# Kernel optimization log

Hardware: AMD Instinct MI355X
Metric: run time of the kernel (lower is better)

Reference implementation:

```python
import jax, jax.numpy as jnp
import numpy as np

N, B, D, K_IN, P = 64, 256, 1792, 35, 10
EPS = 1e-5


def setup_inputs() -> dict:
    key = jax.random.key(0)
    ks = jax.random.split(key, 8)
    s_tok = 1.0 / np.sqrt(K_IN)
    s_net = 1.0 / np.sqrt(D)
    return {
        "X": jax.random.normal(ks[0], (N, B, D), dtype=jnp.float32),
        "task_id": jax.random.normal(ks[1], (B, K_IN), dtype=jnp.float32),
        # tokens: Linear(35, 10*1792)
        "W_tok": jax.random.uniform(ks[2], (P * D, K_IN), jnp.float32, -s_tok, s_tok),
        "b_tok": jax.random.uniform(ks[3], (P * D,), jnp.float32, -s_tok, s_tok),
        # ptokens: Linear(35, 1792)
        "W_ptok": jax.random.uniform(ks[4], (D, K_IN), jnp.float32, -s_tok, s_tok),
        "b_ptok": jax.random.uniform(ks[5], (D,), jnp.float32, -s_tok, s_tok),
        # LayerNorm(1792)
        "gamma": jnp.ones((D,), jnp.float32),
        "beta": jnp.zeros((D,), jnp.float32),
        # net: Linear(1792, 10)
        "W_net": jax.random.uniform(ks[6], (P, D), jnp.float32, -s_net, s_net),
        "b_net": jax.random.uniform(ks[7], (P,), jnp.float32, -s_net, s_net),
    }


def _layernorm(x, gamma, beta):
    mu = jnp.mean(x, axis=-1, keepdims=True)
    var = jnp.mean(jnp.square(x - mu), axis=-1, keepdims=True)
    return (x - mu) * jax.lax.rsqrt(var + EPS) * gamma + beta


def reference(X, task_id, W_tok, b_tok, W_ptok, b_ptok, gamma, beta, W_net, b_net):
    # ptokens(task_id): (b, D); identical across n, so compute once and broadcast.
    ptok = task_id @ W_ptok.T + b_ptok                       # (b, D)
    task_token = _layernorm(ptok[None, :, :] + X, gamma, beta)  # (n, b, D)
    # net -> sigmoid: per-token mixing weights over P prompts.
    weight = jax.nn.sigmoid(task_token @ W_net.T + b_net)    # (n, b, P)
    # tokens(task_id): (b, P, D); identical across n, broadcast in einsum.
    prompt_bank = (task_id @ W_tok.T + b_tok).reshape(B, P, D)  # (b, P, D)
    prompt = jnp.einsum("nbp,bpd->nbd", weight, prompt_bank)  # (n, b, D)
    return X + prompt
```

## Files before the change

kernel.cpp:

```cpp
#include <hip/hip_runtime.h>
#include <hip/hip_bf16.h>

#define NN 64
#define BB 256
#define DD 1792
#define KK 35
#define PP 10
#define DQ 448
#define GR 8
#define NGRP 28

__device__ __forceinline__ float group16_sum_dpp(float x) {
    asm("v_add_f32_dpp %0, %0, %0 row_shr:1 row_mask:0xf bank_mask:0xf bound_ctrl:0" : "+v"(x));
    asm("v_add_f32_dpp %0, %0, %0 row_shr:2 row_mask:0xf bank_mask:0xf bound_ctrl:0" : "+v"(x));
    asm("v_add_f32_dpp %0, %0, %0 row_shr:4 row_mask:0xf bank_mask:0xf bound_ctrl:0" : "+v"(x));
    asm("v_add_f32_dpp %0, %0, %0 row_shr:8 row_mask:0xf bank_mask:0xf bound_ctrl:0" : "+v"(x));
    return x;
}

#define PIN4(v) asm volatile("" : "+v"(v.x), "+v"(v.y), "+v"(v.z), "+v"(v.w))
#define PIN1(s) asm volatile("" : "+v"(s))

__global__ void prep_gf(const float* __restrict__ gamma, const float* __restrict__ beta,
                        const float* __restrict__ Wnet, const float* __restrict__ bnet,
                        float* __restrict__ GF, float* __restrict__ SG, float* __restrict__ ZC) {
    const int p = blockIdx.x;
    const int tid = threadIdx.x;
    float sg = 0.f, sb = 0.f;
#pragma unroll
    for (int j = 0; j < 7; ++j) {
        int d = j * 256 + tid;
        float wv = Wnet[p * DD + d];
        float g = gamma[d] * wv;
        GF[p * DD + d] = g;
        sg += g;
        sb += beta[d] * wv;
    }
#pragma unroll
    for (int off = 32; off > 0; off >>= 1) {
        sg += __shfl_xor(sg, off);
        sb += __shfl_xor(sb, off);
    }
    __shared__ float rs[4][2];
    if ((tid & 63) == 0) { rs[tid >> 6][0] = sg; rs[tid >> 6][1] = sb; }
    __syncthreads();
    if (tid == 0) {
        float a = 0.f, c = 0.f;
#pragma unroll
        for (int w = 0; w < 4; ++w) { a += rs[w][0]; c += rs[w][1]; }
        SG[p] = a;
        ZC[p] = c + bnet[p];
    }
}

__global__ void prep_bank(const float* __restrict__ task,
                          const float* __restrict__ Wtok, const float* __restrict__ btok,
                          const float* __restrict__ Wptok, const float* __restrict__ bptok,
                          float* __restrict__ bank, float* __restrict__ ptok) {
    __shared__ float ti[32 * KK];
    const int tid = threadIdx.x;
    const int b0 = blockIdx.y * 32;
    for (int i = tid; i < 32 * KK; i += 256) ti[i] = task[b0 * KK + i];

    const int r = blockIdx.x * 256 + tid;
    const bool isbank = (r < PP * DD);
    const int rr = isbank ? r : (r - PP * DD);
    const float* __restrict__ W = isbank ? Wtok : Wptok;
    const float bias = isbank ? btok[r] : bptok[rr];

    float w[KK];
#pragma unroll
    for (int k = 0; k < KK; ++k) w[k] = W[rr * KK + k];

    __syncthreads();
#pragma unroll 1
    for (int bb = 0; bb < 32; ++bb) {
        float acc = bias;
#pragma unroll
        for (int k = 0; k < KK; ++k) acc = fmaf(ti[bb * KK + k], w[k], acc);
        const int b = b0 + bb;
        if (isbank) bank[b * (PP * DD) + r] = acc;
        else        ptok[b * DD + rr]       = acc;
    }
}

__global__ __launch_bounds__(448, 1) void fused_lds(
    const float* __restrict__ X, const float* __restrict__ BANK,
    const float* __restrict__ PTOK, const float* __restrict__ GF,
    const float* __restrict__ SG, const float* __restrict__ ZC,
    float* __restrict__ OUT) {
    const int tid  = threadIdx.x;
    const int lane = tid & 63;
    const int c    = tid >> 6;
    const int b    = blockIdx.x;

    const float4* __restrict__ X4 = (const float4*)X;
    const float4* __restrict__ B4 = (const float4*)BANK;
    const float4* __restrict__ G4 = (const float4*)GF;
    const float4* __restrict__ P4 = (const float4*)PTOK;
    float4* __restrict__ O4 = (float4*)OUT;

    __shared__ float xbuf[2][GR][DD];
    __shared__ float red[GR][NGRP][12];
    __shared__ float wlds[GR][PP];

    const size_t rstride = (size_t)BB * DQ;
    const size_t gbase = (size_t)b * DQ + c * 64 + lane;

#define STAGE(BUF, GN)                                                             \
    {                                                                              \
        _Pragma("unroll")                                                          \
        for (int r = 0; r < GR; ++r) {                                             \
            const float4* src = X4 + (size_t)((GN) * GR + r) * rstride + gbase;    \
            __builtin_amdgcn_global_load_lds(                                      \
                (const __attribute__((address_space(1))) void*)src,                \
                (__attribute__((address_space(3))) void*)&xbuf[BUF][r][c * 256],   \
                16, 0, 0);                                                         \
        }                                                                          \
        __builtin_amdgcn_sched_barrier(0);                                         \
    }

    STAGE(0, 0)

    float4 ptk = P4[gbase];
    float4 gf[PP];
#pragma unroll
    for (int p = 0; p < PP; ++p) gf[p] = G4[(size_t)p * DQ + c * 64 + lane];
    float4 bk[PP];
#pragma unroll
    for (int p = 0; p < PP; ++p) bk[p] = B4[((size_t)b * PP + p) * DQ + c * 64 + lane];
    const int vv = tid & 15;
    float sgv = 0.f, zcv = 0.f;
    if (tid < GR * 16 && vv >= 2 && vv < 12) { sgv = SG[vv - 2]; zcv = ZC[vv - 2]; }

    PIN4(ptk);
#pragma unroll
    for (int p = 0; p < PP; ++p) { PIN4(gf[p]); PIN4(bk[p]); }
    PIN1(sgv); PIN1(zcv);

    const bool writer = ((lane & 15) == 15);
    const int g16 = tid >> 4;

#pragma unroll 1
    for (int g = 0; g < 8; ++g) {
        if (g < 7) STAGE((g + 1) & 1, g + 1)

        asm volatile("s_waitcnt vmcnt(8)" ::: "memory");
        __builtin_amdgcn_sched_barrier(0);

        const int cur = g & 1;

#pragma unroll
        for (int r = 0; r < GR; ++r) {
            const float4 x = *(const float4*)&xbuf[cur][r][c * 256 + lane * 4];
            float4 t;
            t.x = x.x + ptk.x; t.y = x.y + ptk.y;
            t.z = x.z + ptk.z; t.w = x.w + ptk.w;

            float s1 = t.x + t.y + t.z + t.w;
            float s2 = t.x * t.x;
            s2 = fmaf(t.y, t.y, s2); s2 = fmaf(t.z, t.z, s2); s2 = fmaf(t.w, t.w, s2);
            float a[PP];
#pragma unroll
            for (int p = 0; p < PP; ++p) {
                float v = t.x * gf[p].x;
                v = fmaf(t.y, gf[p].y, v);
                v = fmaf(t.z, gf[p].z, v);
                v = fmaf(t.w, gf[p].w, v);
                a[p] = v;
            }
            s1 = group16_sum_dpp(s1);
            s2 = group16_sum_dpp(s2);
#pragma unroll
            for (int p = 0; p < PP; ++p) a[p] = group16_sum_dpp(a[p]);

            if (writer) {
                float4* dst = (float4*)&red[r][g16][0];
                dst[0] = make_float4(s1, s2, a[0], a[1]);
                dst[1] = make_float4(a[2], a[3], a[4], a[5]);
                dst[2] = make_float4(a[6], a[7], a[8], a[9]);
            }
        }

        asm volatile("s_waitcnt lgkmcnt(0)" ::: "memory");
        __builtin_amdgcn_sched_barrier(0);
        __builtin_amdgcn_s_barrier();
        __builtin_amdgcn_sched_barrier(0);

        if (tid < GR * 16) {
            const int row = tid >> 4;
            float f = 0.f;
            if (vv < 12) {
#pragma unroll
                for (int q = 0; q < NGRP; ++q) f += red[row][q][vv];
            }
            const int bse = (tid & 63) & ~15;
            const float mu = __shfl(f, bse)     * (1.0f / (float)DD);
            const float ms = __shfl(f, bse + 1) * (1.0f / (float)DD);
            const float istd = rsqrtf(ms - mu * mu + 1e-5f);
            if (vv >= 2 && vv < 12) {
                const float z = istd * (f - mu * sgv) + zcv;
                wlds[row][vv - 2] = 1.0f / (1.0f + __expf(-z));
            }
        }

        asm volatile("s_waitcnt lgkmcnt(0)" ::: "memory");
        __builtin_amdgcn_sched_barrier(0);
        __builtin_amdgcn_s_barrier();
        __builtin_amdgcn_sched_barrier(0);

#pragma unroll
        for (int r = 0; r < GR; ++r) {
            const float4 x = *(const float4*)&xbuf[cur][r][c * 256 + lane * 4];
            float4 acc = x;
#pragma unroll
            for (int p = 0; p < PP; ++p) {
                const float wv = wlds[r][p];
                acc.x = fmaf(wv, bk[p].x, acc.x);
                acc.y = fmaf(wv, bk[p].y, acc.y);
                acc.z = fmaf(wv, bk[p].z, acc.z);
                acc.w = fmaf(wv, bk[p].w, acc.w);
            }
            O4[(size_t)(g * GR + r) * rstride + gbase] = acc;
        }
    }
#undef STAGE
}

extern "C" void kernel_launch(void* const* d_in, const int* in_sizes, int n_in,
                              void* d_out, int out_size, void* d_ws, size_t ws_size,
                              hipStream_t stream) {
    const float* X     = (const float*)d_in[0];
    const float* task  = (const float*)d_in[1];
    const float* Wtok  = (const float*)d_in[2];
    const float* btok  = (const float*)d_in[3];
    const float* Wptok = (const float*)d_in[4];
    const float* bptok = (const float*)d_in[5];
    const float* gamma = (const float*)d_in[6];
    const float* beta  = (const float*)d_in[7];
    const float* Wnet  = (const float*)d_in[8];
    const float* bnet  = (const float*)d_in[9];
    float* out = (float*)d_out;

    float* ws = (float*)d_ws;
    float* bank = ws;
    float* ptok = bank + (size_t)BB * PP * DD;
    float* GF   = ptok + (size_t)BB * DD;
    float* SG   = GF + PP * DD;
    float* ZC   = SG + PP;

    prep_gf<<<PP, 256, 0, stream>>>(gamma, beta, Wnet, bnet, GF, SG, ZC);
    prep_bank<<<dim3(77, 8), 256, 0, stream>>>(task, Wtok, btok, Wptok, bptok, bank, ptok);
    fused_lds<<<BB, 448, 0, stream>>>(X, bank, ptok, GF, SG, ZC, out);
}
```

Baseline: 84.16 us.

## Split fused kernel into a dedicated producer wave and seven consumer waves

Adds an eighth wavefront that only issues the global-to-LDS loads of X for the next row group, while the seven consumer waves compute the layernorm projections, sigmoid weights and output. Synchronisation moves from per-wave vmcnt waits to matched block barriers between producer and consumers. Output stores become nontemporal. The goal is to decouple load issue from compute. In exchange one wave does no arithmetic, and the barrier count per iteration rises.

```diff
diff --git a/kernel.cpp b/kernel.cpp
--- a/kernel.cpp
+++ b/kernel.cpp
@@ -9,6 +9,9 @@
 #define DQ 448
 #define GR 8
 #define NGRP 28
+#define NTH 512
+
+typedef float fx4 __attribute__((ext_vector_type(4)));
 
 __device__ __forceinline__ float group16_sum_dpp(float x) {
     asm("v_add_f32_dpp %0, %0, %0 row_shr:1 row_mask:0xf bank_mask:0xf bound_ctrl:0" : "+v"(x));
@@ -17,9 +20,6 @@
     asm("v_add_f32_dpp %0, %0, %0 row_shr:8 row_mask:0xf bank_mask:0xf bound_ctrl:0" : "+v"(x));
     return x;
 }
-
-#define PIN4(v) asm volatile("" : "+v"(v.x), "+v"(v.y), "+v"(v.z), "+v"(v.w))
-#define PIN1(s) asm volatile("" : "+v"(s))
 
 __global__ void prep_gf(const float* __restrict__ gamma, const float* __restrict__ beta,
                         const float* __restrict__ Wnet, const float* __restrict__ bnet,
@@ -84,146 +84,153 @@
     }
 }
 
-__global__ __launch_bounds__(448, 1) void fused_lds(
+__global__ __launch_bounds__(NTH, 1) void fused_pc(
     const float* __restrict__ X, const float* __restrict__ BANK,
     const float* __restrict__ PTOK, const float* __restrict__ GF,
     const float* __restrict__ SG, const float* __restrict__ ZC,
     float* __restrict__ OUT) {
-    const int tid  = threadIdx.x;
-    const int lane = tid & 63;
-    const int c    = tid >> 6;
-    const int b    = blockIdx.x;
+    const int tid = threadIdx.x;
+    const int b = blockIdx.x;
+    const bool consumer = (tid < 448);
+    const int plane = tid - 448;
 
     const float4* __restrict__ X4 = (const float4*)X;
     const float4* __restrict__ B4 = (const float4*)BANK;
     const float4* __restrict__ G4 = (const float4*)GF;
     const float4* __restrict__ P4 = (const float4*)PTOK;
-    float4* __restrict__ O4 = (float4*)OUT;
+    fx4* __restrict__ OO = (fx4*)OUT;
 
     __shared__ float xbuf[2][GR][DD];
     __shared__ float red[GR][NGRP][12];
     __shared__ float wlds[GR][PP];
 
     const size_t rstride = (size_t)BB * DQ;
-    const size_t gbase = (size_t)b * DQ + c * 64 + lane;
 
 #define STAGE(BUF, GN)                                                             \
     {                                                                              \
         _Pragma("unroll")                                                          \
         for (int r = 0; r < GR; ++r) {                                             \
-            const float4* src = X4 + (size_t)((GN) * GR + r) * rstride + gbase;    \
-            __builtin_amdgcn_global_load_lds(                                      \
-                (const __attribute__((address_space(1))) void*)src,                \
-                (__attribute__((address_space(3))) void*)&xbuf[BUF][r][c * 256],   \
-                16, 0, 0);                                                         \
+            _Pragma("unroll")                                                      \
+            for (int cc = 0; cc < 7; ++cc) {                                       \
+                const float4* src = X4 + (size_t)((GN) * GR + r) * rstride         \
+                                    + (size_t)b * DQ + cc * 64 + plane;            \
+                __builtin_amdgcn_global_load_lds(                                  \
+                    (const __attribute__((address_space(1))) void*)src,            \
+                    (__attribute__((address_space(3))) void*)&xbuf[BUF][r][cc * 256], \
+                    16, 0, 0);                                                     \
+            }                                                                      \
         }                                                                          \
         __builtin_amdgcn_sched_barrier(0);                                         \
     }
 
-    STAGE(0, 0)
-
-    float4 ptk = P4[gbase];
-    float4 gf[PP];
-#pragma unroll
-    for (int p = 0; p < PP; ++p) gf[p] = G4[(size_t)p * DQ + c * 64 + lane];
-    float4 bk[PP];
-#pragma unroll
-    for (int p = 0; p < PP; ++p) bk[p] = B4[((size_t)b * PP + p) * DQ + c * 64 + lane];
+#define BARRIER_RAW()                                                              \
+    asm volatile("s_waitcnt lgkmcnt(0)" ::: "memory");                             \
+    __builtin_amdgcn_sched_barrier(0);                                             \
+    __builtin_amdgcn_s_barrier();                                                  \
+    __builtin_amdgcn_sched_barrier(0);
+
+    float4 ptk = make_float4(0.f, 0.f, 0.f, 0.f);
+    float4 gf[PP], bk[PP];
+    float sgv = 0.f, zcv = 0.f;
     const int vv = tid & 15;
-    float sgv = 0.f, zcv = 0.f;
-    if (tid < GR * 16 && vv >= 2 && vv < 12) { sgv = SG[vv - 2]; zcv = ZC[vv - 2]; }
-
-    PIN4(ptk);
-#pragma unroll
-    for (int p = 0; p < PP; ++p) { PIN4(gf[p]); PIN4(bk[p]); }
-    PIN1(sgv); PIN1(zcv);
-
-    const bool writer = ((lane & 15) == 15);
+    if (consumer) {
+        ptk = P4[(size_t)b * DQ + tid];
+#pragma unroll
+        for (int p = 0; p < PP; ++p) gf[p] = G4[(size_t)p * DQ + tid];
+#pragma unroll
+        for (int p = 0; p < PP; ++p) bk[p] = B4[((size_t)b * PP + p) * DQ + tid];
+        if (tid < GR * 16 && vv >= 2 && vv < 12) { sgv = SG[vv - 2]; zcv = ZC[vv - 2]; }
+    } else {
+        STAGE(0, 0)
+        asm volatile("s_waitcnt vmcnt(0)" ::: "memory");
+    }
+    BARRIER_RAW()
+
+    const bool writer = consumer && ((tid & 15) == 15);
     const int g16 = tid >> 4;
 
 #pragma unroll 1
     for (int g = 0; g < 8; ++g) {
-        if (g < 7) STAGE((g + 1) & 1, g + 1)
-
-        asm volatile("s_waitcnt vmcnt(8)" ::: "memory");
-        __builtin_amdgcn_sched_barrier(0);
-
         const int cur = g & 1;
 
-#pragma unroll
-        for (int r = 0; r < GR; ++r) {
-            const float4 x = *(const float4*)&xbuf[cur][r][c * 256 + lane * 4];
-            float4 t;
-            t.x = x.x + ptk.x; t.y = x.y + ptk.y;
-            t.z = x.z + ptk.z; t.w = x.w + ptk.w;
-
-            float s1 = t.x + t.y + t.z + t.w;
-            float s2 = t.x * t.x;
-            s2 = fmaf(t.y, t.y, s2); s2 = fmaf(t.z, t.z, s2); s2 = fmaf(t.w, t.w, s2);
-            float a[PP];
-#pragma unroll
-            for (int p = 0; p < PP; ++p) {
-                float v = t.x * gf[p].x;
-                v = fmaf(t.y, gf[p].y, v);
-                v = fmaf(t.z, gf[p].z, v);
-                v = fmaf(t.w, gf[p].w, v);
-                a[p] = v;
+        if (consumer) {
+#pragma unroll
+            for (int r = 0; r < GR; ++r) {
+                const float4 x = *(const float4*)&xbuf[cur][r][tid * 4];
+                float4 t;
+                t.x = x.x + ptk.x; t.y = x.y + ptk.y;
+                t.z = x.z + ptk.z; t.w = x.w + ptk.w;
+
+                float s1 = t.x + t.y + t.z + t.w;
+                float s2 = t.x * t.x;
+                s2 = fmaf(t.y, t.y, s2); s2 = fmaf(t.z, t.z, s2); s2 = fmaf(t.w, t.w, s2);
+                float a[PP];
+#pragma unroll
+                for (int p = 0; p < PP; ++p) {
+                    float v = t.x * gf[p].x;
+                    v = fmaf(t.y, gf[p].y, v);
+                    v = fmaf(t.z, gf[p].z, v);
+                    v = fmaf(t.w, gf[p].w, v);
+                    a[p] = v;
+                }
+                s1 = group16_sum_dpp(s1);
+                s2 = group16_sum_dpp(s2);
+#pragma unroll
+                for (int p = 0; p < PP; ++p) a[p] = group16_sum_dpp(a[p]);
+
+                if (writer) {
+                    float4* dst = (float4*)&red[r][g16][0];
+                    dst[0] = make_float4(s1, s2, a[0], a[1]);
+                    dst[1] = make_float4(a[2], a[3], a[4], a[5]);
+                    dst[2] = make_float4(a[6], a[7], a[8], a[9]);
+                }
             }
-            s1 = group16_sum_dpp(s1);
-            s2 = group16_sum_dpp(s2);
-#pragma unroll
-            for (int p = 0; p < PP; ++p) a[p] = group16_sum_dpp(a[p]);
-
-            if (writer) {
-                float4* dst = (float4*)&red[r][g16][0];
-                dst[0] = make_float4(s1, s2, a[0], a[1]);
-                dst[1] = make_float4(a[2], a[3], a[4], a[5]);
-                dst[2] = make_float4(a[6], a[7], a[8], a[9]);
+            BARRIER_RAW()
+
+            if (tid < GR * 16) {
+                const int row = tid >> 4;
+                float f = 0.f;
+                if (vv < 12) {
+#pragma unroll
+                    for (int q = 0; q < NGRP; ++q) f += red[row][q][vv];
+                }
+                const int bse = (tid & 63) & ~15;
+                const float mu = __shfl(f, bse)     * (1.0f / (float)DD);
+                const float ms = __shfl(f, bse + 1) * (1.0f / (float)DD);
+                const float istd = rsqrtf(ms - mu * mu + 1e-5f);
+                if (vv >= 2 && vv < 12) {
+                    const float z = istd * (f - mu * sgv) + zcv;
+                    wlds[row][vv - 2] = 1.0f / (1.0f + __expf(-z));
+                }
             }
+            BARRIER_RAW()
+
+#pragma unroll
+            for (int r = 0; r < GR; ++r) {
+                const float4 x = *(const float4*)&xbuf[cur][r][tid * 4];
+                float4 acc = x;
+#pragma unroll
+                for (int p = 0; p < PP; ++p) {
+                    const float wv = wlds[r][p];
+                    acc.x = fmaf(wv, bk[p].x, acc.x);
+                    acc.y = fmaf(wv, bk[p].y, acc.y);
+                    acc.z = fmaf(wv, bk[p].z, acc.z);
+                    acc.w = fmaf(wv, bk[p].w, acc.w);
+                }
+                fx4 av; av.x = acc.x; av.y = acc.y; av.z = acc.z; av.w = acc.w;
+                __builtin_nontemporal_store(av,
+                    &OO[(size_t)(g * GR + r) * rstride + (size_t)b * DQ + tid]);
+            }
+            BARRIER_RAW()
+        } else {
+            if (g < 7) STAGE(cur ^ 1, g + 1)
+            BARRIER_RAW()
+            BARRIER_RAW()
+            asm volatile("s_waitcnt vmcnt(0)" ::: "memory");
+            BARRIER_RAW()
         }
-
-        asm volatile("s_waitcnt lgkmcnt(0)" ::: "memory");
-        __builtin_amdgcn_sched_barrier(0);
-        __builtin_amdgcn_s_barrier();
-        __builtin_amdgcn_sched_barrier(0);
-
-        if (tid < GR * 16) {
-            const int row = tid >> 4;
-            float f = 0.f;
-            if (vv < 12) {
-#pragma unroll
-                for (int q = 0; q < NGRP; ++q) f += red[row][q][vv];
-            }
-            const int bse = (tid & 63) & ~15;
-            const float mu = __shfl(f, bse)     * (1.0f / (float)DD);
-            const float ms = __shfl(f, bse + 1) * (1.0f / (float)DD);
-            const float istd = rsqrtf(ms - mu * mu + 1e-5f);
-            if (vv >= 2 && vv < 12) {
-                const float z = istd * (f - mu * sgv) + zcv;
-                wlds[row][vv - 2] = 1.0f / (1.0f + __expf(-z));
-            }
-        }
-
-        asm volatile("s_waitcnt lgkmcnt(0)" ::: "memory");
-        __builtin_amdgcn_sched_barrier(0);
-        __builtin_amdgcn_s_barrier();
-        __builtin_amdgcn_sched_barrier(0);
-
-#pragma unroll
-        for (int r = 0; r < GR; ++r) {
-            const float4 x = *(const float4*)&xbuf[cur][r][c * 256 + lane * 4];
-            float4 acc = x;
-#pragma unroll
-            for (int p = 0; p < PP; ++p) {
-                const float wv = wlds[r][p];
-                acc.x = fmaf(wv, bk[p].x, acc.x);
-                acc.y = fmaf(wv, bk[p].y, acc.y);
-                acc.z = fmaf(wv, bk[p].z, acc.z);
-                acc.w = fmaf(wv, bk[p].w, acc.w);
-            }
-            O4[(size_t)(g * GR + r) * rstride + gbase] = acc;
-        }
-    }
+    }
+#undef BARRIER_RAW
 #undef STAGE
 }
 
@@ -251,5 +258,5 @@
 
     prep_gf<<<PP, 256, 0, stream>>>(gamma, beta, Wnet, bnet, GF, SG, ZC);
     prep_bank<<<dim3(77, 8), 256, 0, stream>>>(task, Wtok, btok, Wptok, bptok, bank, ptok);
-    fused_lds<<<BB, 448, 0, stream>>>(X, bank, ptok, GF, SG, ZC, out);
-}
+    fused_pc<<<BB, NTH, 0, stream>>>(X, bank, ptok, GF, SG, ZC, out);
+}
```

After: 78.84 us. 1.07x faster.
